# Kernel optimization log

Measured on AMD Instinct MI355X. Metric: run time of the kernel, lower is better.

Reference implementation:

```python
import jax, jax.numpy as jnp
import numpy as np

N, E = 100000, 1600000
NFEAT, NHID, NCLASS, NLAYER = 128, 128, 40, 3


def _glorot(key, shape):
    fan_in, fan_out = shape[0], shape[1]
    lim = float(np.sqrt(6.0 / (fan_in + fan_out)))
    return jax.random.uniform(key, shape, jnp.float32, -lim, lim)


def setup_inputs() -> dict:
    key = jax.random.key(0)
    ks = jax.random.split(key, 12)
    x = jax.random.normal(ks[0], (N, NFEAT), jnp.float32)
    src = jax.random.randint(ks[1], (E,), 0, N, jnp.int32)
    dst = jax.random.randint(ks[2], (E,), 0, N, jnp.int32)
    W1 = _glorot(ks[3], (NFEAT, NHID)); b1 = jnp.zeros((NHID,), jnp.float32)
    W2 = _glorot(ks[4], (NHID, NHID)); b2 = jnp.zeros((NHID,), jnp.float32)
    Wg = jnp.stack([_glorot(ks[5 + l], (NHID, NHID)) for l in range(NLAYER)])  # [L,H,H]
    bg = jnp.zeros((NLAYER, NHID), jnp.float32)
    Wc = _glorot(ks[5 + NLAYER], (NHID, NCLASS)); bc = jnp.zeros((NCLASS,), jnp.float32)
    return {"x": x, "src": src, "dst": dst, "W1": W1, "b1": b1, "W2": W2,
            "b2": b2, "Wg": Wg, "bg": bg, "Wc": Wc, "bc": bc}


def _graph_conv(h, src, dst, W, b, out_norm, in_norm):
    # DGL GraphConv norm='both': scale by src out-deg^{-1/2}, sum-aggregate,
    # scale by dst in-deg^{-1/2}, then linear (in_feats == out_feats -> W after agg).
    h = h * out_norm[:, None]
    agg = jax.ops.segment_sum(h[src], dst, num_segments=N)
    return (agg * in_norm[:, None]) @ W + b


def reference(x, src, dst, W1, b1, W2, b2, Wg, bg, Wc, bc):
    ones = jnp.ones((E,), jnp.float32)
    out_deg = jnp.clip(jax.ops.segment_sum(ones, src, num_segments=N), 1.0)
    in_deg = jnp.clip(jax.ops.segment_sum(ones, dst, num_segments=N), 1.0)
    out_norm = jax.lax.rsqrt(out_deg)
    in_norm = jax.lax.rsqrt(in_deg)

    h = x @ W1 + b1            # feature1
    h = h @ W2 + b2            # feature2
    for l in range(NLAYER):    # stacked GraphConv + ReLU (dropout is identity in eval)
        h = _graph_conv(h, src, dst, Wg[l], bg[l], out_norm, in_norm)
        h = jax.nn.relu(h)
    return h @ Wc + bc         # classifier
```

## Files before the change

### kernel.cpp

```cpp
#include <hip/hip_runtime.h>
#include <hip/hip_fp16.h>
#include <cstdint>
#include <cstddef>

constexpr int NN  = 100000;
constexpr int EE  = 1600000;
constexpr int HID = 128;
constexpr int BUK = 256;
constexpr int NBUK = (NN + BUK - 1) / BUK;
constexpr int BLKE = 2048;
constexpr int NBE  = (EE + BLKE - 1) / BLKE;
constexpr int MH   = NBUK * NBE;
constexpr int NSC  = (MH + 1023) / 1024;

typedef float f32x4_t __attribute__((ext_vector_type(4)));
typedef short bf16x8_t __attribute__((ext_vector_type(8)));

static __device__ __forceinline__ short f2bf(float f) {
    union { float f; unsigned u; } x; x.f = f;
    unsigned r = x.u + 0x7FFF + ((x.u >> 16) & 1);
    return (short)(r >> 16);
}
static __device__ __forceinline__ float bf2f(short b) {
    union { unsigned u; float f; } x; x.u = ((unsigned)(unsigned short)b) << 16;
    return x.f;
}

__global__ __launch_bounds__(256) void deg_zero_k(int* __restrict__ outdeg) {
    int i = blockIdx.x * 256 + threadIdx.x;
    if (i < NN) outdeg[i] = 0;
}

__global__ __launch_bounds__(256) void bh_d_k(const int* __restrict__ src, const int* __restrict__ dst,
                                              int* __restrict__ bh_d, int* __restrict__ outdeg) {
    __shared__ int hd[NBUK];
    int blk = blockIdx.x, t = threadIdx.x;
    for (int i = t; i < NBUK; i += 256) hd[i] = 0;
    __syncthreads();
    int e0 = blk * BLKE, e1 = min(e0 + BLKE, EE);
    for (int e = e0 + t; e < e1; e += 256) {
        atomicAdd(&hd[dst[e] >> 8], 1);
        atomicAdd(&outdeg[src[e]], 1);
    }
    __syncthreads();
    for (int i = t; i < NBUK; i += 256) bh_d[i * NBE + blk] = hd[i];
}

__global__ __launch_bounds__(256) void onorm_k(const int* __restrict__ outdeg, float* __restrict__ onorm) {
    int i = blockIdx.x * 256 + threadIdx.x;
    if (i < NN) {
        int c = outdeg[i]; if (c < 1) c = 1;
        onorm[i] = rsqrtf((float)c);
    }
}

__global__ __launch_bounds__(256) void scan_sum_k(const int* __restrict__ in, int* __restrict__ bsum, int n) {
    __shared__ int sc[256];
    int b = blockIdx.x, t = threadIdx.x;
    int base = b * 1024 + t * 4;
    int s = 0;
#pragma unroll
    for (int j = 0; j < 4; j++) { int idx = base + j; s += (idx < n) ? in[idx] : 0; }
    sc[t] = s; __syncthreads();
    for (int off = 128; off > 0; off >>= 1) {
        if (t < off) sc[t] += sc[t + off];
        __syncthreads();
    }
    if (t == 0) bsum[b] = sc[0];
}

__global__ __launch_bounds__(512) void scan_top_k(const int* __restrict__ bsum, int* __restrict__ boff, int nb) {
    __shared__ int sc[512];
    int t = threadIdx.x;
    int v = (t < nb) ? bsum[t] : 0;
    sc[t] = v; __syncthreads();
    for (int off = 1; off < 512; off <<= 1) {
        int u = (t >= off) ? sc[t - off] : 0;
        __syncthreads();
        sc[t] += u;
        __syncthreads();
    }
    if (t < nb) boff[t] = sc[t] - v;
}

__global__ __launch_bounds__(256) void scan_chunk_k(const int* __restrict__ in, const int* __restrict__ boff,
                                                    int* __restrict__ out, int n) {
    __shared__ int sc[256];
    int b = blockIdx.x, t = threadIdx.x;
    int base = b * 1024 + t * 4;
    int c[4];
#pragma unroll
    for (int j = 0; j < 4; j++) { int idx = base + j; c[j] = (idx < n) ? in[idx] : 0; }
    int s = c[0] + c[1] + c[2] + c[3];
    sc[t] = s; __syncthreads();
    for (int off = 1; off < 256; off <<= 1) {
        int v = (t >= off) ? sc[t - off] : 0;
        __syncthreads();
        sc[t] += v;
        __syncthreads();
    }
    int excl = sc[t] - s + boff[b];
#pragma unroll
    for (int j = 0; j < 4; j++) {
        int idx = base + j;
        if (idx < n) out[idx] = excl;
        excl += c[j];
    }
}

__global__ __launch_bounds__(256) void scatter_d_k(const int* __restrict__ src, const int* __restrict__ dst,
                                                   const int* __restrict__ off_d, unsigned* __restrict__ pairs) {
    __shared__ int cd[NBUK];
    int blk = blockIdx.x, t = threadIdx.x;
    for (int i = t; i < NBUK; i += 256) cd[i] = off_d[i * NBE + blk];
    __syncthreads();
    int e0 = blk * BLKE, e1 = min(e0 + BLKE, EE);
    for (int e = e0 + t; e < e1; e += 256) {
        int d = dst[e], s = src[e];
        int pd = atomicAdd(&cd[d >> 8], 1);
        pairs[pd] = ((unsigned)(d & 255) << 17) | (unsigned)s;
    }
}

__global__ __launch_bounds__(512) void bucket_csr_k(const unsigned* __restrict__ pairs, const int* __restrict__ off_d,
                                                    int* __restrict__ rowptr, int* __restrict__ col,
                                                    float* __restrict__ inorm) {
    __shared__ int hist[BUK];
    __shared__ int excl[BUK];
    __shared__ int psum[BUK];
    int b = blockIdx.x, t = threadIdx.x;
    int base = off_d[b * NBE];
    int endv = (b == NBUK - 1) ? EE : off_d[(b + 1) * NBE];
    if (t < BUK) hist[t] = 0;
    __syncthreads();
    for (int i = base + t; i < endv; i += 512) atomicAdd(&hist[pairs[i] >> 17], 1);
    __syncthreads();
    int ps = 0;
    if (t < BUK) { ps = hist[t]; psum[t] = ps; }
    __syncthreads();
    for (int off = 1; off < BUK; off <<= 1) {
        int u = 0;
        if (t < BUK && t >= off) u = psum[t - off];
        __syncthreads();
        if (t < BUK) psum[t] += u;
        __syncthreads();
    }
    if (t < BUK) {
        int pex = psum[t] - ps;
        excl[t] = pex;
        int node = b * BUK + t;
        if (node < NN) {
            rowptr[node] = base + pex;
            int c = ps; if (c < 1) c = 1;
            inorm[node] = rsqrtf((float)c);
        }
    }
    if (b == NBUK - 1 && t == 0) rowptr[NN] = EE;
    __syncthreads();
    for (int i = base + t; i < endv; i += 512) {
        unsigned p = pairs[i];
        int pos = base + atomicAdd(&excl[p >> 17], 1);
        col[pos] = (int)(p & 0x1FFFFu);
    }
}

__global__ __launch_bounds__(256) void w12_k(const float* __restrict__ W1, const float* __restrict__ W2,
                                             const float* __restrict__ b1, const float* __restrict__ b2,
                                             float* __restrict__ W12, float* __restrict__ b12) {
    if (blockIdx.x == 64) {
        int j = threadIdx.x;
        if (j < 128) {
            float acc = b2[j];
            for (int k = 0; k < 128; k++) acc = fmaf(b1[k], W2[k * 128 + j], acc);
            b12[j] = acc;
        }
        return;
    }
    int idx = blockIdx.x * 256 + threadIdx.x;
    int i = idx >> 7, j = idx & 127;
    float a0 = 0.f, a1 = 0.f, a2 = 0.f, a3 = 0.f;
    for (int k = 0; k < 128; k += 4) {
        a0 = fmaf(W1[i * 128 + k],     W2[(k)     * 128 + j], a0);
        a1 = fmaf(W1[i * 128 + k + 1], W2[(k + 1) * 128 + j], a1);
        a2 = fmaf(W1[i * 128 + k + 2], W2[(k + 2) * 128 + j], a2);
        a3 = fmaf(W1[i * 128 + k + 3], W2[(k + 3) * 128 + j], a3);
    }
    W12[idx] = (a0 + a1) + (a2 + a3);
}

__global__ __launch_bounds__(256) void agg_k(const float4* __restrict__ h16, const int* __restrict__ rowptr,
                                             const int* __restrict__ col, float4* __restrict__ out) {
    int w = (int)((blockIdx.x * 256 + threadIdx.x) >> 6);
    if (w >= NN) return;
    int lane = threadIdx.x & 63;
    int q   = lane >> 4;
    int l16 = lane & 15;
    int beg = rowptr[w], end = rowptr[w + 1];
    float acc[8];
#pragma unroll
    for (int j = 0; j < 8; j++) acc[j] = 0.f;

    const char* hb = (const char*)h16 + (size_t)l16 * 16;
    union HU { float4 f4; __half2 h2[4]; };
    int i = beg + q;
    for (; i + 12 < end; i += 16) {
        int s0 = __builtin_nontemporal_load(col + i);
        int s1 = __builtin_nontemporal_load(col + i + 4);
        int s2 = __builtin_nontemporal_load(col + i + 8);
        int s3 = __builtin_nontemporal_load(col + i + 12);
        HU u0, u1, u2, u3;
        u0.f4 = *(const float4*)(hb + (unsigned)s0 * 256u);
        u1.f4 = *(const float4*)(hb + (unsigned)s1 * 256u);
        u2.f4 = *(const float4*)(hb + (unsigned)s2 * 256u);
        u3.f4 = *(const float4*)(hb + (unsigned)s3 * 256u);
#pragma unroll
        for (int p = 0; p < 4; p++) {
            float2 a = __half22float2(u0.h2[p]);
            float2 b = __half22float2(u1.h2[p]);
            float2 c = __half22float2(u2.h2[p]);
            float2 d = __half22float2(u3.h2[p]);
            acc[2 * p]     += (a.x + b.x) + (c.x + d.x);
            acc[2 * p + 1] += (a.y + b.y) + (c.y + d.y);
        }
    }
    for (; i < end; i += 4) {
        int s = __builtin_nontemporal_load(col + i);
        HU u; u.f4 = *(const float4*)(hb + (unsigned)s * 256u);
#pragma unroll
        for (int p = 0; p < 4; p++) {
            float2 a = __half22float2(u.h2[p]);
            acc[2 * p]     += a.x;
            acc[2 * p + 1] += a.y;
        }
    }
#pragma unroll
    for (int mm = 16; mm <= 32; mm <<= 1)
#pragma unroll
        for (int j = 0; j < 8; j++) acc[j] += __shfl_xor(acc[j], mm);
    if (q == 0) {
        f32x4_t o0 = {acc[0], acc[1], acc[2], acc[3]};
        f32x4_t o1 = {acc[4], acc[5], acc[6], acc[7]};
        __builtin_nontemporal_store(o0, (f32x4_t*)&out[(size_t)w * 32 + l16 * 2]);
        __builtin_nontemporal_store(o1, (f32x4_t*)&out[(size_t)w * 32 + l16 * 2 + 1]);
    }
}

template <int NT, bool RELU, bool INSCALE, bool OUTSCALE, bool OUTHALF>
__global__ __launch_bounds__(256) void mfma_gemm_k(
    const float* __restrict__ in, const float* __restrict__ inscale,
    const float* __restrict__ W, const float* __restrict__ bias,
    void* __restrict__ outp, const float* __restrict__ outscale,
    int nrows, int ncols, int ngroups) {

    __shared__ short Bh[NT * 2048];
    __shared__ short Bl[NT * 2048];

    const int t = threadIdx.x;

    if constexpr (NT == 8) {
        for (int j = 0; j < 16; j++) {
            int fi = (j * 256 + t) * 4;
            int k = fi >> 7, n0 = fi & 127;
            float4 wv = *(const float4*)(W + fi);
            float wa[4] = {wv.x, wv.y, wv.z, wv.w};
#pragma unroll
            for (int c = 0; c < 4; c++) {
                int n = n0 + c;
                int nt = n >> 4, kblk = k >> 5, ksub = k & 31;
                int lane_ = ((ksub >> 3) << 4) | (n & 15);
                int sidx = ((nt * 4 + kblk) * 64 + lane_) * 8 + (ksub & 7);
                short hi = f2bf(wa[c]);
                short lo = f2bf(wa[c] - bf2f(hi));
                Bh[sidx] = hi; Bl[sidx] = lo;
            }
        }
    } else {
        for (int idx = t; idx < 128 * 64; idx += 256) {
            int k = idx >> 6, n = idx & 63;
            if (n < NT * 16) {
                float w = (n < 40) ? W[k * 40 + n] : 0.f;
                int nt = n >> 4, kblk = k >> 5, ksub = k & 31;
                int lane_ = ((ksub >> 3) << 4) | (n & 15);
                int sidx = ((nt * 4 + kblk) * 64 + lane_) * 8 + (ksub & 7);
                short hi = f2bf(w);
                short lo = f2bf(w - bf2f(hi));
                Bh[sidx] = hi; Bl[sidx] = lo;
            }
        }
    }
    __syncthreads();

    const int wave = t >> 6;
    const int lane = t & 63;
    const int m    = lane & 15;
    const int kq   = lane >> 4;

    for (int g = blockIdx.x; g < ngroups; g += gridDim.x) {
        int grow0 = g * 64 + wave * 16;
        int row   = grow0 + m;
        bool rv   = row < nrows;

        bf16x8_t Ah[4], Al[4];
        float s = 1.f;
        if (INSCALE && rv) s = inscale[row];
#pragma unroll
        for (int kb = 0; kb < 4; kb++) {
            const float* ap = in + (size_t)row * 128 + kb * 32 + kq * 8;
            f32x4_t p0, p1;
            if (rv) {
                p0 = __builtin_nontemporal_load((const f32x4_t*)ap);
                p1 = __builtin_nontemporal_load((const f32x4_t*)(ap + 4));
            } else {
                p0 = (f32x4_t){0.f, 0.f, 0.f, 0.f};
                p1 = (f32x4_t){0.f, 0.f, 0.f, 0.f};
            }
            float av[8] = {p0.x, p0.y, p0.z, p0.w, p1.x, p1.y, p1.z, p1.w};
#pragma unroll
            for (int j = 0; j < 8; j++) {
                float v = INSCALE ? av[j] * s : av[j];
                short hi = f2bf(v);
                Ah[kb][j] = hi;
                Al[kb][j] = f2bf(v - bf2f(hi));
            }
        }

        int crow0 = grow0 + kq * 4;
        float osr[4];
#pragma unroll
        for (int r = 0; r < 4; r++) {
            int crow = crow0 + r;
            osr[r] = (OUTSCALE && crow < nrows) ? outscale[crow] : 1.f;
        }

#pragma unroll
        for (int nt = 0; nt < NT; nt++) {
            f32x4_t acc = {0.f, 0.f, 0.f, 0.f};
#pragma unroll
            for (int kb = 0; kb < 4; kb++) {
                const bf16x8_t bh = *(const bf16x8_t*)&Bh[((nt * 4 + kb) * 64 + lane) * 8];
                const bf16x8_t bl = *(const bf16x8_t*)&Bl[((nt * 4 + kb) * 64 + lane) * 8];
                acc = __builtin_amdgcn_mfma_f32_16x16x32_bf16(Ah[kb], bh, acc, 0, 0, 0);
                acc = __builtin_amdgcn_mfma_f32_16x16x32_bf16(Al[kb], bh, acc, 0, 0, 0);
                acc = __builtin_amdgcn_mfma_f32_16x16x32_bf16(Ah[kb], bl, acc, 0, 0, 0);
            }
            int ccol = nt * 16 + m;
            bool cv = (NT == 8) ? true : (ccol < ncols);
            float bv = cv ? bias[ccol] : 0.f;
#pragma unroll
            for (int r = 0; r < 4; r++) {
                int crow = crow0 + r;
                if (crow < nrows && cv) {
                    float v = acc[r] + bv;
                    if (RELU) v = fmaxf(v, 0.f);
                    v *= osr[r];
                    if (OUTHALF) ((__half*)outp)[(size_t)crow * ncols + ccol] = __float2half_rn(v);
                    else         ((float*)outp)[(size_t)crow * ncols + ccol] = v;
                }
            }
        }
    }
}

extern "C" void kernel_launch(void* const* d_in, const int* in_sizes, int n_in,
                              void* d_out, int out_size, void* d_ws, size_t ws_size,
                              hipStream_t stream) {
    const float* x   = (const float*)d_in[0];
    const int*   src = (const int*)d_in[1];
    const int*   dst = (const int*)d_in[2];
    const float* W1  = (const float*)d_in[3];
    const float* b1  = (const float*)d_in[4];
    const float* W2  = (const float*)d_in[5];
    const float* b2  = (const float*)d_in[6];
    const float* Wg  = (const float*)d_in[7];
    const float* bg  = (const float*)d_in[8];
    const float* Wc  = (const float*)d_in[9];
    const float* bc  = (const float*)d_in[10];
    float* out = (float*)d_out;

    char* ws = (char*)d_ws;
    size_t off = 0;
    auto alloc = [&](size_t bytes) -> void* {
        void* p = ws + off;
        off += (bytes + 255) & ~(size_t)255;
        return p;
    };
    float*  h0     = (float*)alloc((size_t)NN * HID * 4);
    float*  h1     = (float*)alloc((size_t)NN * HID * 4);
    __half* h16    = (__half*)alloc((size_t)NN * HID * 2);
    float*  W12    = (float*)alloc(128 * 128 * 4);
    float*  b12    = (float*)alloc(128 * 4);
    float*  onorm  = (float*)alloc((size_t)NN * 4);
    float*  inorm  = (float*)alloc((size_t)NN * 4);
    int*    outdeg = (int*)alloc((size_t)NN * 4);
    int*    rowptr = (int*)alloc((size_t)(NN + 1) * 4);
    int*    col    = (int*)alloc((size_t)EE * 4);
    int*    bh_d   = (int*)alloc((size_t)MH * 4);
    int*    off_d  = (int*)alloc((size_t)MH * 4);
    int*    bsum   = (int*)alloc((size_t)NSC * 4);
    int*    boff   = (int*)alloc((size_t)NSC * 4);
    unsigned* pairs = (unsigned*)h0;

    deg_zero_k<<<(NN + 255) / 256, 256, 0, stream>>>(outdeg);
    bh_d_k<<<NBE, 256, 0, stream>>>(src, dst, bh_d, outdeg);
    onorm_k<<<(NN + 255) / 256, 256, 0, stream>>>(outdeg, onorm);
    scan_sum_k<<<NSC, 256, 0, stream>>>(bh_d, bsum, MH);
    scan_top_k<<<1, 512, 0, stream>>>(bsum, boff, NSC);
    scan_chunk_k<<<NSC, 256, 0, stream>>>(bh_d, boff, off_d, MH);
    scatter_d_k<<<NBE, 256, 0, stream>>>(src, dst, off_d, pairs);
    bucket_csr_k<<<NBUK, 512, 0, stream>>>(pairs, off_d, rowptr, col, inorm);

    w12_k<<<65, 256, 0, stream>>>(W1, W2, b1, b2, W12, b12);

    const int ngroups = (NN + 63) / 64;
    const int ggrid   = 512;

    mfma_gemm_k<8, false, false, true, true><<<ggrid, 256, 0, stream>>>(
        x, nullptr, W12, b12, h16, onorm, NN, 128, ngroups);
    for (int l = 0; l < 3; l++) {
        agg_k<<<(NN * 64 + 255) / 256, 256, 0, stream>>>(
            (const float4*)h16, rowptr, col, (float4*)h0);
        if (l < 2) {
            mfma_gemm_k<8, true, true, true, true><<<ggrid, 256, 0, stream>>>(
                h0, inorm, Wg + (size_t)l * 128 * 128, bg + (size_t)l * 128, h16, onorm, NN, 128, ngroups);
        } else {
            mfma_gemm_k<8, true, true, false, false><<<ggrid, 256, 0, stream>>>(
                h0, inorm, Wg + (size_t)l * 128 * 128, bg + (size_t)l * 128, h1, nullptr, NN, 128, ngroups);
        }
    }
    mfma_gemm_k<3, false, false, false, false><<<ggrid, 256, 0, stream>>>(
        h1, nullptr, Wc, bc, out, nullptr, NN, 40, ngroups);
}
```

Measured before the change: 624.6 us.

## Compute out-degree via bucketed counting sort instead of global atomics

Replaces per-edge global atomicAdd on the out-degree array with a second bucketed histogram and scatter on src, writing low-byte keys into a scratch buffer. A per-bucket shared-memory histogram then produces onorm inside the CSR-build kernel through extra blocks. This targets contended, scattered global atomics and drops two small kernels. In exchange it adds a second three-kernel scan pass, a 1.6M-byte scatter, and larger per-block histogram arrays.

```diff
diff --git a/kernel.cpp b/kernel.cpp
--- a/kernel.cpp
+++ b/kernel.cpp
@@ -26,31 +26,21 @@
     return x.f;
 }
 
-__global__ __launch_bounds__(256) void deg_zero_k(int* __restrict__ outdeg) {
-    int i = blockIdx.x * 256 + threadIdx.x;
-    if (i < NN) outdeg[i] = 0;
-}
-
-__global__ __launch_bounds__(256) void bh_d_k(const int* __restrict__ src, const int* __restrict__ dst,
-                                              int* __restrict__ bh_d, int* __restrict__ outdeg) {
-    __shared__ int hd[NBUK];
+__global__ __launch_bounds__(256) void bh_both_k(const int* __restrict__ src, const int* __restrict__ dst,
+                                                 int* __restrict__ bh_d, int* __restrict__ bh_s) {
+    __shared__ int hd[NBUK], hs[NBUK];
     int blk = blockIdx.x, t = threadIdx.x;
-    for (int i = t; i < NBUK; i += 256) hd[i] = 0;
+    for (int i = t; i < NBUK; i += 256) { hd[i] = 0; hs[i] = 0; }
     __syncthreads();
     int e0 = blk * BLKE, e1 = min(e0 + BLKE, EE);
     for (int e = e0 + t; e < e1; e += 256) {
         atomicAdd(&hd[dst[e] >> 8], 1);
-        atomicAdd(&outdeg[src[e]], 1);
-    }
-    __syncthreads();
-    for (int i = t; i < NBUK; i += 256) bh_d[i * NBE + blk] = hd[i];
-}
-
-__global__ __launch_bounds__(256) void onorm_k(const int* __restrict__ outdeg, float* __restrict__ onorm) {
-    int i = blockIdx.x * 256 + threadIdx.x;
-    if (i < NN) {
-        int c = outdeg[i]; if (c < 1) c = 1;
-        onorm[i] = rsqrtf((float)c);
+        atomicAdd(&hs[src[e] >> 8], 1);
+    }
+    __syncthreads();
+    for (int i = t; i < NBUK; i += 256) {
+        bh_d[i * NBE + blk] = hd[i];
+        bh_s[i * NBE + blk] = hs[i];
     }
 }
 
@@ -108,27 +98,55 @@
     }
 }
 
-__global__ __launch_bounds__(256) void scatter_d_k(const int* __restrict__ src, const int* __restrict__ dst,
-                                                   const int* __restrict__ off_d, unsigned* __restrict__ pairs) {
-    __shared__ int cd[NBUK];
+__global__ __launch_bounds__(256) void scatter_both_k(const int* __restrict__ src, const int* __restrict__ dst,
+                                                      const int* __restrict__ off_d, const int* __restrict__ off_s,
+                                                      unsigned* __restrict__ pairs, unsigned char* __restrict__ sbyte) {
+    __shared__ int cd[NBUK], cs[NBUK];
     int blk = blockIdx.x, t = threadIdx.x;
-    for (int i = t; i < NBUK; i += 256) cd[i] = off_d[i * NBE + blk];
+    for (int i = t; i < NBUK; i += 256) {
+        cd[i] = off_d[i * NBE + blk];
+        cs[i] = off_s[i * NBE + blk];
+    }
     __syncthreads();
     int e0 = blk * BLKE, e1 = min(e0 + BLKE, EE);
     for (int e = e0 + t; e < e1; e += 256) {
         int d = dst[e], s = src[e];
         int pd = atomicAdd(&cd[d >> 8], 1);
         pairs[pd] = ((unsigned)(d & 255) << 17) | (unsigned)s;
-    }
-}
-
-__global__ __launch_bounds__(512) void bucket_csr_k(const unsigned* __restrict__ pairs, const int* __restrict__ off_d,
-                                                    int* __restrict__ rowptr, int* __restrict__ col,
-                                                    float* __restrict__ inorm) {
+        int ps = atomicAdd(&cs[s >> 8], 1);
+        sbyte[ps] = (unsigned char)(s & 255);
+    }
+}
+
+__global__ __launch_bounds__(512) void bucket_csr_ocnt_k(
+    const unsigned* __restrict__ pairs, const int* __restrict__ off_d,
+    const unsigned char* __restrict__ sbyte, const int* __restrict__ off_s,
+    int* __restrict__ rowptr, int* __restrict__ col,
+    float* __restrict__ inorm, float* __restrict__ onorm) {
     __shared__ int hist[BUK];
     __shared__ int excl[BUK];
     __shared__ int psum[BUK];
-    int b = blockIdx.x, t = threadIdx.x;
+    int t = threadIdx.x;
+
+    if (blockIdx.x >= NBUK) {
+        int b = blockIdx.x - NBUK;
+        int base = off_s[b * NBE];
+        int endv = (b == NBUK - 1) ? EE : off_s[(b + 1) * NBE];
+        if (t < BUK) hist[t] = 0;
+        __syncthreads();
+        for (int i = base + t; i < endv; i += 512) atomicAdd(&hist[sbyte[i]], 1);
+        __syncthreads();
+        if (t < BUK) {
+            int node = b * BUK + t;
+            if (node < NN) {
+                int c = hist[t]; if (c < 1) c = 1;
+                onorm[node] = rsqrtf((float)c);
+            }
+        }
+        return;
+    }
+
+    int b = blockIdx.x;
     int base = off_d[b * NBE];
     int endv = (b == NBUK - 1) ? EE : off_d[(b + 1) * NBE];
     if (t < BUK) hist[t] = 0;
@@ -391,23 +409,27 @@
     float*  b12    = (float*)alloc(128 * 4);
     float*  onorm  = (float*)alloc((size_t)NN * 4);
     float*  inorm  = (float*)alloc((size_t)NN * 4);
-    int*    outdeg = (int*)alloc((size_t)NN * 4);
     int*    rowptr = (int*)alloc((size_t)(NN + 1) * 4);
     int*    col    = (int*)alloc((size_t)EE * 4);
     int*    bh_d   = (int*)alloc((size_t)MH * 4);
+    int*    bh_s   = (int*)alloc((size_t)MH * 4);
     int*    off_d  = (int*)alloc((size_t)MH * 4);
+    int*    off_s  = (int*)alloc((size_t)MH * 4);
     int*    bsum   = (int*)alloc((size_t)NSC * 4);
     int*    boff   = (int*)alloc((size_t)NSC * 4);
-    unsigned* pairs = (unsigned*)h0;
-
-    deg_zero_k<<<(NN + 255) / 256, 256, 0, stream>>>(outdeg);
-    bh_d_k<<<NBE, 256, 0, stream>>>(src, dst, bh_d, outdeg);
-    onorm_k<<<(NN + 255) / 256, 256, 0, stream>>>(outdeg, onorm);
+    unsigned*      pairs = (unsigned*)h0;
+    unsigned char* sbyte = (unsigned char*)h0 + (size_t)EE * 4;
+
+    bh_both_k<<<NBE, 256, 0, stream>>>(src, dst, bh_d, bh_s);
     scan_sum_k<<<NSC, 256, 0, stream>>>(bh_d, bsum, MH);
     scan_top_k<<<1, 512, 0, stream>>>(bsum, boff, NSC);
     scan_chunk_k<<<NSC, 256, 0, stream>>>(bh_d, boff, off_d, MH);
-    scatter_d_k<<<NBE, 256, 0, stream>>>(src, dst, off_d, pairs);
-    bucket_csr_k<<<NBUK, 512, 0, stream>>>(pairs, off_d, rowptr, col, inorm);
+    scan_sum_k<<<NSC, 256, 0, stream>>>(bh_s, bsum, MH);
+    scan_top_k<<<1, 512, 0, stream>>>(bsum, boff, NSC);
+    scan_chunk_k<<<NSC, 256, 0, stream>>>(bh_s, boff, off_s, MH);
+    scatter_both_k<<<NBE, 256, 0, stream>>>(src, dst, off_d, off_s, pairs, sbyte);
+    bucket_csr_ocnt_k<<<2 * NBUK, 512, 0, stream>>>(pairs, off_d, sbyte, off_s,
+                                                    rowptr, col, inorm, onorm);
 
     w12_k<<<65, 256, 0, stream>>>(W1, W2, b1, b2, W12, b12);
 
```

New measurement: 589.4 us. 5.6% less time.
